# Optimization experiments

Measured on AMD Instinct MI355X. Metric: run time of the kernel, lower is better.

Reference implementation:

```python
import jax, jax.numpy as jnp
import numpy as np


def _rigid_matrix(p1, p2, w):
    # p1, p2: [B, N, 3]; w: [B, 1, N] (weights summing to 1 over N)
    p1 = jnp.swapaxes(p1, 1, 2)  # [B,3,N]
    p2 = jnp.swapaxes(p2, 1, 2)
    p1_c = jnp.sum(p1 * w, axis=2, keepdims=True)  # weighted centroid [B,3,1]
    p2_c = jnp.sum(p2 * w, axis=2, keepdims=True)
    q1 = (p1 - p1_c) * w
    q2 = (p2 - p2_c) * w
    Hm = jnp.einsum('bin,bjn->bij', q1, q2)  # [B,3,3] cross-covariance
    U, _, Vt = jnp.linalg.svd(Hm, full_matrices=False)
    V = jnp.swapaxes(Vt, 1, 2)
    Ut = jnp.swapaxes(U, 1, 2)
    R = V @ Ut
    det = jnp.linalg.det(R)  # [B]
    s = jnp.sign(det)
    # original scales the third ROW of V by sign(det) (rows [1,1,sign])
    scale = jnp.stack([jnp.ones_like(s), jnp.ones_like(s), s], axis=1)[:, :, None]  # [B,3,1]
    V = V * scale
    R = V @ Ut
    T = p2_c - R @ p1_c  # [B,3,1]
    return jnp.concatenate([R, T], axis=-1)  # [B,3,4]


def _affine_grid_3d(theta, D, H, W):
    # matches torch F.affine_grid(theta, (B,C,D,H,W), align_corners=False)
    def coords(n):
        return (2.0 * jnp.arange(n, dtype=theta.dtype) + 1.0) / n - 1.0
    zs, ys, xs = coords(D), coords(H), coords(W)
    Z, Y, X = jnp.meshgrid(zs, ys, xs, indexing='ij')
    base = jnp.stack([X, Y, Z], axis=-1)  # [D,H,W,3], last dim = (x,y,z)
    grid = jnp.einsum('dhwj,bij->bdhwi', base, theta[:, :, :3])
    grid = grid + theta[:, None, None, None, :, 3]
    return grid  # [B,D,H,W,3]


def setup_inputs() -> dict:
    key = jax.random.key(0)
    k1, k2, k3 = jax.random.split(key, 3)
    B, N = 4, 128
    points_m = jax.random.normal(k1, (B, N, 3), jnp.float32) * 0.5
    points_f = jax.random.normal(k2, (B, N, 3), jnp.float32) * 0.5
    w = jax.random.uniform(k3, (B, 1, N), jnp.float32)
    weights = w / jnp.sum(w, axis=-1, keepdims=True)  # normalized -> valid centroid weights
    return {"points_m": points_m, "points_f": points_f, "weights": weights,
            "D": 160, "H": 192, "W": 160}


def reference(points_m, points_f, weights, D, H, W):
    # forward = grid_from_points: matrix = get_matrix(points_f, points_m, w)
    theta = _rigid_matrix(points_f, points_m, weights)
    return _affine_grid_3d(theta, D, H, W)
```

## Files before the change

kernel.cpp:

```cpp
#include <hip/hip_runtime.h>
#include <math.h>

#define B_ 4
#define N_ 128
#define D_ 160
#define H_ 192
#define W_ 160

__global__ __launch_bounds__(256) void rigid_kernel(const float* __restrict__ pm,
                                                    const float* __restrict__ pf,
                                                    const float* __restrict__ wt,
                                                    float* __restrict__ theta) {
  __shared__ float bc[B_][15];
  const int tid = threadIdx.x;
  const int b = tid >> 6;
  const int lane = tid & 63;

  const int base = b * N_;
  float wA = wt[base + lane], wB = wt[base + lane + 64];
  float fA[3], fB[3], mA[3], mB[3];
#pragma unroll
  for (int c = 0; c < 3; ++c) {
    fA[c] = pf[(base + lane) * 3 + c];
    fB[c] = pf[(base + lane + 64) * 3 + c];
    mA[c] = pm[(base + lane) * 3 + c];
    mB[c] = pm[(base + lane + 64) * 3 + c];
  }

  float sums[6];
#pragma unroll
  for (int c = 0; c < 3; ++c) {
    sums[c]     = wA * fA[c] + wB * fB[c];
    sums[3 + c] = wA * mA[c] + wB * mB[c];
  }
#pragma unroll
  for (int k = 0; k < 6; ++k) {
    float v = sums[k];
#pragma unroll
    for (int o = 1; o < 64; o <<= 1) v += __shfl_xor(v, o, 64);
    sums[k] = v;
  }

  float q1A[3], q1B[3], q2A[3], q2B[3];
#pragma unroll
  for (int c = 0; c < 3; ++c) {
    q1A[c] = (fA[c] - sums[c]) * wA;     q1B[c] = (fB[c] - sums[c]) * wB;
    q2A[c] = (mA[c] - sums[3 + c]) * wA; q2B[c] = (mB[c] - sums[3 + c]) * wB;
  }
  float Hm[9];
#pragma unroll
  for (int i = 0; i < 3; ++i)
#pragma unroll
    for (int j = 0; j < 3; ++j)
      Hm[i * 3 + j] = q1A[i] * q2A[j] + q1B[i] * q2B[j];
#pragma unroll
  for (int k = 0; k < 9; ++k) {
    float v = Hm[k];
#pragma unroll
    for (int o = 1; o < 64; o <<= 1) v += __shfl_xor(v, o, 64);
    Hm[k] = v;
  }

  if (lane == 0) {
#pragma unroll
    for (int k = 0; k < 6; ++k) bc[b][k] = sums[k];
#pragma unroll
    for (int k = 0; k < 9; ++k) bc[b][6 + k] = Hm[k];
  }
  __syncthreads();

  if (tid < B_) {
    const int bb = tid;
    double X[3][3];
    double fr = 0.0;
    for (int i = 0; i < 3; ++i)
      for (int j = 0; j < 3; ++j) {
        X[i][j] = (double)bc[bb][6 + i * 3 + j];
        fr += X[i][j] * X[i][j];
      }
    fr = sqrt(fr);
    if (fr < 1e-300) fr = 1.0;
    for (int i = 0; i < 3; ++i)
      for (int j = 0; j < 3; ++j) X[i][j] /= fr;

    for (int it = 0; it < 12; ++it) {
      double C[3][3];
      C[0][0] =  X[1][1] * X[2][2] - X[1][2] * X[2][1];
      C[0][1] = -(X[1][0] * X[2][2] - X[1][2] * X[2][0]);
      C[0][2] =  X[1][0] * X[2][1] - X[1][1] * X[2][0];
      C[1][0] = -(X[0][1] * X[2][2] - X[0][2] * X[2][1]);
      C[1][1] =  X[0][0] * X[2][2] - X[0][2] * X[2][0];
      C[1][2] = -(X[0][0] * X[2][1] - X[0][1] * X[2][0]);
      C[2][0] =  X[0][1] * X[1][2] - X[0][2] * X[1][1];
      C[2][1] = -(X[0][0] * X[1][2] - X[0][2] * X[1][0]);
      C[2][2] =  X[0][0] * X[1][1] - X[0][1] * X[1][0];
      double det = X[0][0] * C[0][0] + X[0][1] * C[0][1] + X[0][2] * C[0][2];
      double ad = fabs(det);
      double mu = (ad > 1e-300 && ad < 1e300) ? pow(ad, -1.0 / 3.0) : 1.0;
      double inv = 1.0 / (mu * det);
      for (int i = 0; i < 3; ++i)
        for (int j = 0; j < 3; ++j)
          X[i][j] = 0.5 * (mu * X[i][j] + C[i][j] * inv);
    }

    double R[3][3];
    for (int i = 0; i < 3; ++i)
      for (int j = 0; j < 3; ++j) R[i][j] = X[j][i];

    double det = R[0][0] * (R[1][1] * R[2][2] - R[1][2] * R[2][1])
               - R[0][1] * (R[1][0] * R[2][2] - R[1][2] * R[2][0])
               + R[0][2] * (R[1][0] * R[2][1] - R[1][1] * R[2][0]);
    double s = (det < 0.0) ? -1.0 : 1.0;
    R[2][0] *= s; R[2][1] *= s; R[2][2] *= s;

    const double c1d[3] = {bc[bb][0], bc[bb][1], bc[bb][2]};
    const double c2d[3] = {bc[bb][3], bc[bb][4], bc[bb][5]};
    for (int i = 0; i < 3; ++i) {
      double Ti = c2d[i] - (R[i][0] * c1d[0] + R[i][1] * c1d[1] + R[i][2] * c1d[2]);
      theta[bb * 12 + i * 4 + 0] = (float)R[i][0];
      theta[bb * 12 + i * 4 + 1] = (float)R[i][1];
      theta[bb * 12 + i * 4 + 2] = (float)R[i][2];
      theta[bb * 12 + i * 4 + 3] = (float)Ti;
    }
  }
}

__global__ __launch_bounds__(256) void grid_kernel(const float* __restrict__ theta,
                                                   float4* __restrict__ out) {
  const int F_PER_ROW = (W_ * 3) / 4;
  const int f = blockIdx.x * 256 + threadIdx.x;

  const int row = f / F_PER_ROW;
  const int lf4 = f - row * F_PER_ROW;
  const int h = row % H_;
  const int rd = row / H_;
  const int d = rd % D_;
  const int b = rd / D_;

  const int lf = lf4 * 4;
  const int w0 = lf / 3;
  const int phase = lf - 3 * w0;

  const float y = (2.0f * (float)h + 1.0f) * (1.0f / (float)H_) - 1.0f;
  const float z = (2.0f * (float)d + 1.0f) * (1.0f / (float)D_) - 1.0f;
  const float x0 = (2.0f * (float)w0 + 1.0f) * (1.0f / (float)W_) - 1.0f;

  const float4* thv = (const float4*)(theta + b * 12);
  const float4 r0 = thv[0];
  const float4 r1 = thv[1];
  const float4 r2 = thv[2];

  const float A0 = fmaf(r0.x, x0, fmaf(r0.y, y, fmaf(r0.z, z, r0.w)));
  const float A1 = fmaf(r1.x, x0, fmaf(r1.y, y, fmaf(r1.z, z, r1.w)));
  const float A2 = fmaf(r2.x, x0, fmaf(r2.y, y, fmaf(r2.z, z, r2.w)));
  const float dx = 2.0f / (float)W_;
  const float B0 = fmaf(r0.x, dx, A0);
  const float B1 = fmaf(r1.x, dx, A1);
  const float B2 = fmaf(r2.x, dx, A2);

  float4 o;
  o.x = (phase == 0) ? A0 : ((phase == 1) ? A1 : A2);
  o.y = (phase == 0) ? A1 : ((phase == 1) ? A2 : B0);
  o.z = (phase == 0) ? A2 : ((phase == 1) ? B0 : B1);
  o.w = (phase == 0) ? B0 : ((phase == 1) ? B1 : B2);

  out[f] = o;
}

extern "C" void kernel_launch(void* const* d_in, const int* in_sizes, int n_in,
                              void* d_out, int out_size, void* d_ws, size_t ws_size,
                              hipStream_t stream) {
  const float* pm = (const float*)d_in[0];
  const float* pf = (const float*)d_in[1];
  const float* wt = (const float*)d_in[2];
  float* theta = (float*)d_ws;
  float4* out = (float4*)d_out;

  rigid_kernel<<<1, 256, 0, stream>>>(pm, pf, wt, theta);

  const int nF4 = B_ * D_ * H_ * W_ * 3 / 4;
  grid_kernel<<<nF4 / 256, 256, 0, stream>>>(theta, out);
}
```

Measured before the change: 50.12 us.

## Make grid threads write multiple vectors with nontemporal stores; trim polar iterations

```diff
diff --git a/kernel.cpp b/kernel.cpp
--- a/kernel.cpp
+++ b/kernel.cpp
@@ -6,6 +6,8 @@
 #define D_ 160
 #define H_ 192
 #define W_ 160
+
+typedef float floatx4 __attribute__((ext_vector_type(4)));
 
 __global__ __launch_bounds__(256) void rigid_kernel(const float* __restrict__ pm,
                                                     const float* __restrict__ pf,
@@ -83,7 +85,7 @@
     for (int i = 0; i < 3; ++i)
       for (int j = 0; j < 3; ++j) X[i][j] /= fr;
 
-    for (int it = 0; it < 12; ++it) {
+    for (int it = 0; it < 9; ++it) {
       double C[3][3];
       C[0][0] =  X[1][1] * X[2][2] - X[1][2] * X[2][1];
       C[0][1] = -(X[1][0] * X[2][2] - X[1][2] * X[2][0]);
@@ -95,8 +97,10 @@
       C[2][1] = -(X[0][0] * X[1][2] - X[0][2] * X[1][0]);
       C[2][2] =  X[0][0] * X[1][1] - X[0][1] * X[1][0];
       double det = X[0][0] * C[0][0] + X[0][1] * C[0][1] + X[0][2] * C[0][2];
-      double ad = fabs(det);
-      double mu = (ad > 1e-300 && ad < 1e300) ? pow(ad, -1.0 / 3.0) : 1.0;
+      float adf = fabsf((float)det);
+      float muf = (adf > 1e-30f && adf < 1e30f)
+                      ? exp2f(log2f(adf) * (-1.0f / 3.0f)) : 1.0f;
+      double mu = (double)muf;
       double inv = 1.0 / (mu * det);
       for (int i = 0; i < 3; ++i)
         for (int j = 0; j < 3; ++j)
@@ -125,46 +129,53 @@
   }
 }
 
+#define F_PER_ROW ((W_ * 3) / 4)
+#define F4_TOTAL (B_ * D_ * H_ * F_PER_ROW)
+#define BLOCKS_PER_BATCH 1800
+
 __global__ __launch_bounds__(256) void grid_kernel(const float* __restrict__ theta,
-                                                   float4* __restrict__ out) {
-  const int F_PER_ROW = (W_ * 3) / 4;
-  const int f = blockIdx.x * 256 + threadIdx.x;
+                                                   floatx4* __restrict__ out) {
+  const int tid = threadIdx.x;
+  const int blk = blockIdx.x;
+  const int b = blk / BLOCKS_PER_BATCH;
 
-  const int row = f / F_PER_ROW;
-  const int lf4 = f - row * F_PER_ROW;
-  const int h = row % H_;
-  const int rd = row / H_;
-  const int d = rd % D_;
-  const int b = rd / D_;
+  const float* th = theta + b * 12;
+  const float r00 = th[0], r01 = th[1], r02 = th[2],  t0 = th[3];
+  const float r10 = th[4], r11 = th[5], r12 = th[6],  t1 = th[7];
+  const float r20 = th[8], r21 = th[9], r22 = th[10], t2 = th[11];
+  const float dx = 2.0f / (float)W_;
 
-  const int lf = lf4 * 4;
-  const int w0 = lf / 3;
-  const int phase = lf - 3 * w0;
+  int f = blk * 2048 + tid;
+#pragma unroll
+  for (int k = 0; k < 8; ++k, f += 256) {
+    const int row = f / F_PER_ROW;
+    const int lf4 = f - row * F_PER_ROW;
+    const int h = row % H_;
+    const int d = (row / H_) % D_;
 
-  const float y = (2.0f * (float)h + 1.0f) * (1.0f / (float)H_) - 1.0f;
-  const float z = (2.0f * (float)d + 1.0f) * (1.0f / (float)D_) - 1.0f;
-  const float x0 = (2.0f * (float)w0 + 1.0f) * (1.0f / (float)W_) - 1.0f;
+    const int lf = lf4 * 4;
+    const int w0 = lf / 3;
+    const int phase = lf - 3 * w0;
 
-  const float4* thv = (const float4*)(theta + b * 12);
-  const float4 r0 = thv[0];
-  const float4 r1 = thv[1];
-  const float4 r2 = thv[2];
+    const float y = (2.0f * (float)h + 1.0f) * (1.0f / (float)H_) - 1.0f;
+    const float z = (2.0f * (float)d + 1.0f) * (1.0f / (float)D_) - 1.0f;
+    const float x0 = (2.0f * (float)w0 + 1.0f) * (1.0f / (float)W_) - 1.0f;
 
-  const float A0 = fmaf(r0.x, x0, fmaf(r0.y, y, fmaf(r0.z, z, r0.w)));
-  const float A1 = fmaf(r1.x, x0, fmaf(r1.y, y, fmaf(r1.z, z, r1.w)));
-  const float A2 = fmaf(r2.x, x0, fmaf(r2.y, y, fmaf(r2.z, z, r2.w)));
-  const float dx = 2.0f / (float)W_;
-  const float B0 = fmaf(r0.x, dx, A0);
-  const float B1 = fmaf(r1.x, dx, A1);
-  const float B2 = fmaf(r2.x, dx, A2);
+    const float A0 = fmaf(r00, x0, fmaf(r01, y, fmaf(r02, z, t0)));
+    const float A1 = fmaf(r10, x0, fmaf(r11, y, fmaf(r12, z, t1)));
+    const float A2 = fmaf(r20, x0, fmaf(r21, y, fmaf(r22, z, t2)));
+    const float B0 = fmaf(r00, dx, A0);
+    const float B1 = fmaf(r10, dx, A1);
+    const float B2 = fmaf(r20, dx, A2);
 
-  float4 o;
-  o.x = (phase == 0) ? A0 : ((phase == 1) ? A1 : A2);
-  o.y = (phase == 0) ? A1 : ((phase == 1) ? A2 : B0);
-  o.z = (phase == 0) ? A2 : ((phase == 1) ? B0 : B1);
-  o.w = (phase == 0) ? B0 : ((phase == 1) ? B1 : B2);
+    floatx4 o;
+    o.x = (phase == 0) ? A0 : ((phase == 1) ? A1 : A2);
+    o.y = (phase == 0) ? A1 : ((phase == 1) ? A2 : B0);
+    o.z = (phase == 0) ? A2 : ((phase == 1) ? B0 : B1);
+    o.w = (phase == 0) ? B0 : ((phase == 1) ? B1 : B2);
 
-  out[f] = o;
+    __builtin_nontemporal_store(o, out + f);
+  }
 }
 
 extern "C" void kernel_launch(void* const* d_in, const int* in_sizes, int n_in,
@@ -174,10 +185,10 @@
   const float* pf = (const float*)d_in[1];
   const float* wt = (const float*)d_in[2];
   float* theta = (float*)d_ws;
-  float4* out = (float4*)d_out;
+  floatx4* out = (floatx4*)d_out;
 
   rigid_kernel<<<1, 256, 0, stream>>>(pm, pf, wt, theta);
 
-  const int nF4 = B_ * D_ * H_ * W_ * 3 / 4;
-  grid_kernel<<<nF4 / 256, 256, 0, stream>>>(theta, out);
+  const int nBlocks = F4_TOTAL / 2048;
+  grid_kernel<<<nBlocks, 256, 0, stream>>>(theta, out);
 }
```

Result: slower. 52.58 us (+4.9%).
